# Performance work log

Hardware: AMD Instinct MI355X
Metric: run time of the kernel (lower is better)

## Reference

```python
import jax, jax.numpy as jnp
import numpy as np

N, TD, TE, D = 8, 1024, 2048, 1024

def setup_inputs() -> dict:
    key = jax.random.key(0)
    kq, km, kl = jax.random.split(key, 3)
    queries = jax.random.normal(kq, (N, TD, D), dtype=jnp.float32)
    memory = jax.random.normal(km, (N, TE, D), dtype=jnp.float32)
    # lengths in [1, TE] so no row is fully masked (avoids NaN softmax)
    lengths = jax.random.randint(kl, (N,), 1, TE + 1, dtype=jnp.int32)
    return {"queries": queries, "memory": memory, "lengths": lengths}

def reference(queries, memory, lengths):
    scale = jnp.asarray(np.sqrt(D), dtype=queries.dtype)
    # [N, Td, Te] = bmm(queries, memory^T) / sqrt(D)
    weights = jnp.einsum('ntd,nsd->nts', queries, memory) / scale
    # padding mask: position s is invalid if s >= lengths[n]
    mask = jnp.arange(TE)[None, :] >= lengths[:, None]          # [N, Te]
    weights = jnp.where(mask[:, None, :], -jnp.inf, weights)
    alignments = jax.nn.softmax(weights, axis=-1)               # [N, Td, Te]
    contexts = jnp.einsum('nts,nsd->ntd', alignments, memory)   # [N, Td, D]
    return (contexts, alignments)
```

## Files before the change

### kernel.cpp

```cpp
#include <hip/hip_runtime.h>
#include <hip/hip_bf16.h>

#define NB 8
#define TDIM 1024
#define TEDIM 2048
#define DDIM 1024

typedef __bf16 bf16x8 __attribute__((ext_vector_type(8)));
typedef float f32x4 __attribute__((ext_vector_type(4)));
typedef unsigned short us8 __attribute__((ext_vector_type(8)));

static __device__ __forceinline__ void gld_lds16(const __bf16* g, __bf16* l) {
    __builtin_amdgcn_global_load_lds(
        (const __attribute__((address_space(1))) void*)g,
        (__attribute__((address_space(3))) void*)l,
        16, 0, 0);
}

static __device__ __forceinline__ unsigned short bf16_bits(float f) {
    __bf16 h = (__bf16)f;
    return __builtin_bit_cast(unsigned short, h);
}
static __device__ __forceinline__ float bits_f32(unsigned short u) {
    return (float)__builtin_bit_cast(__bf16, u);
}

__global__ __launch_bounds__(256) void cast_bf16_kernel(
    const float* __restrict__ src, __bf16* __restrict__ dst)
{
    const size_t i = ((size_t)blockIdx.x * 256 + threadIdx.x) * 8;
    float4 a = *reinterpret_cast<const float4*>(&src[i]);
    float4 b = *reinterpret_cast<const float4*>(&src[i + 4]);
    us8 o;
    o[0] = bf16_bits(a.x); o[1] = bf16_bits(a.y);
    o[2] = bf16_bits(a.z); o[3] = bf16_bits(a.w);
    o[4] = bf16_bits(b.x); o[5] = bf16_bits(b.y);
    o[6] = bf16_bits(b.z); o[7] = bf16_bits(b.w);
    *reinterpret_cast<us8*>(&dst[i]) = o;
}

__global__ __launch_bounds__(256) void transpose_cast_m_kernel(
    const float* __restrict__ M, __bf16* __restrict__ Mb,
    __bf16* __restrict__ Mt)
{
    const int n  = blockIdx.z;
    const int s0 = blockIdx.x * 64;
    const int d0 = blockIdx.y * 64;
    const float* Mn  = M  + (size_t)n * TEDIM * DDIM;
    __bf16*      Mbn = Mb + (size_t)n * TEDIM * DDIM;
    __bf16*      Mtn = Mt + (size_t)n * DDIM * TEDIM;

    __shared__ float tile[64][65];
    const int t = threadIdx.x;

    #pragma unroll
    for (int j = 0; j < 4; ++j) {
        const int flat = j * 256 + t;
        const int r  = flat >> 4;
        const int c4 = (flat & 15) * 4;
        float4 v = *reinterpret_cast<const float4*>(
            &Mn[(size_t)(s0 + r) * DDIM + d0 + c4]);
        tile[r][c4 + 0] = v.x; tile[r][c4 + 1] = v.y;
        tile[r][c4 + 2] = v.z; tile[r][c4 + 3] = v.w;
        ushort4 o;
        o.x = bf16_bits(v.x); o.y = bf16_bits(v.y);
        o.z = bf16_bits(v.z); o.w = bf16_bits(v.w);
        *reinterpret_cast<ushort4*>(&Mbn[(size_t)(s0 + r) * DDIM + d0 + c4]) = o;
    }
    __syncthreads();

    const int dr  = t >> 2;
    const int sc0 = (t & 3) * 16;
    us8 o0, o1;
    #pragma unroll
    for (int i = 0; i < 8; ++i)  o0[i] = bf16_bits(tile[sc0 + i][dr]);
    #pragma unroll
    for (int i = 0; i < 8; ++i)  o1[i] = bf16_bits(tile[sc0 + 8 + i][dr]);
    __bf16* dst = &Mtn[(size_t)(d0 + dr) * TEDIM + s0 + sc0];
    *reinterpret_cast<us8*>(dst)     = o0;
    *reinterpret_cast<us8*>(dst + 8) = o1;
}

template<int LDA, int LDB, int LDC, int KDIM, int GX, int GY, int GR,
         bool SCALE, bool OUTBF16>
__global__ __launch_bounds__(256) void gemm_bt_kernel(
    const __bf16* __restrict__ A, const __bf16* __restrict__ B,
    void* __restrict__ Cv)
{
    constexpr int PER_B = GX * GY;
    const int L   = blockIdx.x + GX * (blockIdx.y + GY * blockIdx.z);
    const int n   = L & 7;
    const int rem = L >> 3;
    const int rg  = rem / (GR * GY);
    const int r2  = rem % (GR * GY);
    const int row0 = (rg * GR + (r2 % GR)) * 128;
    const int col0 = (r2 / GR) * 128;

    const __bf16* Ab = A + (size_t)n * GX * 128 * LDA + (size_t)row0 * LDA;
    const __bf16* Bb = B + (size_t)n * GY * 128 * LDB + (size_t)col0 * LDB;

    __shared__ __align__(16) __bf16 As[128 * 32];
    __shared__ __align__(16) __bf16 Bs[128 * 32];

    const int t    = threadIdx.x;
    const int lane = t & 63;
    const int w    = t >> 6;
    const int wr   = (w >> 1) * 64;
    const int wc   = (w & 1) * 64;

    f32x4 acc[4][4] = {};

    for (int k0 = 0; k0 < KDIM; k0 += 32) {
        #pragma unroll
        for (int j = 0; j < 2; ++j) {
            const int tt = j * 256 + t;
            const int r  = tt >> 2;
            const int c  = (tt & 3) * 8;
            gld_lds16(Ab + (size_t)r * LDA + k0 + c, &As[tt * 8]);
            gld_lds16(Bb + (size_t)r * LDB + k0 + c, &Bs[tt * 8]);
        }
        __syncthreads();

        bf16x8 af[4], bfr[4];
        #pragma unroll
        for (int i = 0; i < 4; ++i)
            af[i] = *reinterpret_cast<const bf16x8*>(
                &As[(wr + i * 16 + (lane & 15)) * 32 + (lane >> 4) * 8]);
        #pragma unroll
        for (int j = 0; j < 4; ++j)
            bfr[j] = *reinterpret_cast<const bf16x8*>(
                &Bs[(wc + j * 16 + (lane & 15)) * 32 + (lane >> 4) * 8]);

        #pragma unroll
        for (int i = 0; i < 4; ++i)
            #pragma unroll
            for (int j = 0; j < 4; ++j)
                acc[i][j] = __builtin_amdgcn_mfma_f32_16x16x32_bf16(
                    af[i], bfr[j], acc[i][j], 0, 0, 0);
        __syncthreads();
    }

    const float sc = SCALE ? 0.03125f : 1.0f;
    #pragma unroll
    for (int i = 0; i < 4; ++i) {
        #pragma unroll
        for (int j = 0; j < 4; ++j) {
            const int col   = col0 + wc + j * 16 + (lane & 15);
            const int rbase = row0 + wr + i * 16 + (lane >> 4) * 4;
            #pragma unroll
            for (int r = 0; r < 4; ++r) {
                const size_t idx =
                    (size_t)n * GX * 128 * LDC + (size_t)(rbase + r) * LDC + col;
                if constexpr (OUTBF16)
                    ((__bf16*)Cv)[idx] = (__bf16)(acc[i][j][r] * sc);
                else
                    ((float*)Cv)[idx] = acc[i][j][r] * sc;
            }
        }
    }
}

__global__ __launch_bounds__(256) void softmax_kernel(
    __bf16* __restrict__ P, float* __restrict__ Sout,
    const int* __restrict__ len_p)
{
    const int row = blockIdx.x;
    const int n   = row >> 10;
    const int len = len_p[n];
    __bf16* Pr = P    + (size_t)row * TEDIM;
    float*  Sr = Sout + (size_t)row * TEDIM;

    const int t    = threadIdx.x;
    const int lane = t & 63;
    const int w    = t >> 6;
    const int s0   = t * 8;

    us8 raw = *reinterpret_cast<const us8*>(&Pr[s0]);
    float v[8];
    #pragma unroll
    for (int i = 0; i < 8; ++i) {
        v[i] = bits_f32(raw[i]);
        if (s0 + i >= len) v[i] = -INFINITY;
    }

    float mx = v[0];
    #pragma unroll
    for (int i = 1; i < 8; ++i) mx = fmaxf(mx, v[i]);
    #pragma unroll
    for (int off = 32; off; off >>= 1) mx = fmaxf(mx, __shfl_xor(mx, off));

    __shared__ float redm[4], reds[4];
    if (lane == 0) redm[w] = mx;
    __syncthreads();
    mx = fmaxf(fmaxf(redm[0], redm[1]), fmaxf(redm[2], redm[3]));

    float e[8];
    float sum = 0.f;
    #pragma unroll
    for (int i = 0; i < 8; ++i) { e[i] = __expf(v[i] - mx); sum += e[i]; }
    #pragma unroll
    for (int off = 32; off; off >>= 1) sum += __shfl_xor(sum, off);
    if (lane == 0) reds[w] = sum;
    __syncthreads();
    sum = reds[0] + reds[1] + reds[2] + reds[3];

    const float r = 1.0f / sum;
    float p[8];
    #pragma unroll
    for (int i = 0; i < 8; ++i) p[i] = e[i] * r;

    float4 oa = {p[0], p[1], p[2], p[3]};
    float4 ob = {p[4], p[5], p[6], p[7]};
    *reinterpret_cast<float4*>(&Sr[s0])     = oa;
    *reinterpret_cast<float4*>(&Sr[s0 + 4]) = ob;

    us8 o;
    #pragma unroll
    for (int i = 0; i < 8; ++i) o[i] = bf16_bits(p[i]);
    *reinterpret_cast<us8*>(&Pr[s0]) = o;
}

extern "C" void kernel_launch(void* const* d_in, const int* in_sizes, int n_in,
                              void* d_out, int out_size, void* d_ws, size_t ws_size,
                              hipStream_t stream) {
    const float* Q       = (const float*)d_in[0];
    const float* M       = (const float*)d_in[1];
    const int*   lengths = (const int*)d_in[2];

    float* ctx   = (float*)d_out;
    float* align = ctx + (size_t)NB * TDIM * DDIM;

    __bf16* Qb = (__bf16*)d_ws;
    __bf16* Mb = Qb + (size_t)NB * TDIM * DDIM;
    __bf16* Mt = Mb + (size_t)NB * TEDIM * DDIM;
    __bf16* Pb = Mt + (size_t)NB * DDIM * TEDIM;

    dim3 blk(256);
    cast_bf16_kernel<<<dim3(NB * TDIM * DDIM / (8 * 256)), blk, 0, stream>>>(Q, Qb);
    transpose_cast_m_kernel<<<dim3(TEDIM / 64, DDIM / 64, NB), blk, 0, stream>>>(M, Mb, Mt);
    gemm_bt_kernel<DDIM, DDIM, TEDIM, DDIM, 8, 16, 8, true, true>
        <<<dim3(8, 16, NB), blk, 0, stream>>>(Qb, Mb, (void*)Pb);
    softmax_kernel<<<dim3(NB * TDIM), blk, 0, stream>>>(Pb, align, lengths);
    gemm_bt_kernel<TEDIM, TEDIM, DDIM, TEDIM, 8, 8, 4, false, false>
        <<<dim3(8, 8, NB), blk, 0, stream>>>(Pb, Mt, (void*)ctx);
}
```

Before: 296.3 us.

## Skip masked key positions in transpose, scores and context GEMMs

Uses the per-batch lengths to skip work on padded memory positions. The transpose/cast kernel skips 64-row tiles beyond the length. The scores GEMM returns early for 128-column tiles past the length, with a column remap that interleaves low and high tiles to spread the surviving blocks. The context GEMM limits its K loop to the length rounded up to 32. Correctness depends on softmax overwriting masked positions with -inf and then writing zero probabilities there, because the skipped regions of the workspace are left unwritten.

```diff
diff --git a/kernel.cpp b/kernel.cpp
--- a/kernel.cpp
+++ b/kernel.cpp
@@ -41,10 +41,11 @@
 
 __global__ __launch_bounds__(256) void transpose_cast_m_kernel(
     const float* __restrict__ M, __bf16* __restrict__ Mb,
-    __bf16* __restrict__ Mt)
+    __bf16* __restrict__ Mt, const int* __restrict__ len_p)
 {
     const int n  = blockIdx.z;
     const int s0 = blockIdx.x * 64;
+    if (s0 >= len_p[n]) return;
     const int d0 = blockIdx.y * 64;
     const float* Mn  = M  + (size_t)n * TEDIM * DDIM;
     __bf16*      Mbn = Mb + (size_t)n * TEDIM * DDIM;
@@ -81,23 +82,21 @@
     *reinterpret_cast<us8*>(dst + 8) = o1;
 }
 
-template<int LDA, int LDB, int LDC, int KDIM, int GX, int GY, int GR,
-         bool SCALE, bool OUTBF16>
-__global__ __launch_bounds__(256) void gemm_bt_kernel(
-    const __bf16* __restrict__ A, const __bf16* __restrict__ B,
-    void* __restrict__ Cv)
-{
-    constexpr int PER_B = GX * GY;
-    const int L   = blockIdx.x + GX * (blockIdx.y + GY * blockIdx.z);
-    const int n   = L & 7;
-    const int rem = L >> 3;
-    const int rg  = rem / (GR * GY);
-    const int r2  = rem % (GR * GY);
-    const int row0 = (rg * GR + (r2 % GR)) * 128;
-    const int col0 = (r2 / GR) * 128;
-
-    const __bf16* Ab = A + (size_t)n * GX * 128 * LDA + (size_t)row0 * LDA;
-    const __bf16* Bb = B + (size_t)n * GY * 128 * LDB + (size_t)col0 * LDB;
+__global__ __launch_bounds__(256) void scores_kernel(
+    const __bf16* __restrict__ Qb, const __bf16* __restrict__ Mb,
+    __bf16* __restrict__ Pb, const int* __restrict__ len_p)
+{
+    const int n   = blockIdx.z;
+    const int len = len_p[n];
+    const int xc  = blockIdx.x;
+    const int ct  = (xc < 8) ? xc : 23 - xc;
+    const int col0 = ct * 128;
+    if (col0 >= len) return;
+    const int row0 = blockIdx.y * 128;
+
+    const __bf16* Ab = Qb + (size_t)n * TDIM * DDIM + (size_t)row0 * DDIM;
+    const __bf16* Bb = Mb + (size_t)n * TEDIM * DDIM + (size_t)col0 * DDIM;
+    __bf16*       Cb = Pb + (size_t)n * TDIM * TEDIM;
 
     __shared__ __align__(16) __bf16 As[128 * 32];
     __shared__ __align__(16) __bf16 Bs[128 * 32];
@@ -110,14 +109,14 @@
 
     f32x4 acc[4][4] = {};
 
-    for (int k0 = 0; k0 < KDIM; k0 += 32) {
+    for (int k0 = 0; k0 < DDIM; k0 += 32) {
         #pragma unroll
         for (int j = 0; j < 2; ++j) {
             const int tt = j * 256 + t;
             const int r  = tt >> 2;
             const int c  = (tt & 3) * 8;
-            gld_lds16(Ab + (size_t)r * LDA + k0 + c, &As[tt * 8]);
-            gld_lds16(Bb + (size_t)r * LDB + k0 + c, &Bs[tt * 8]);
+            gld_lds16(Ab + (size_t)r * DDIM + k0 + c, &As[tt * 8]);
+            gld_lds16(Bb + (size_t)r * DDIM + k0 + c, &Bs[tt * 8]);
         }
         __syncthreads();
 
@@ -140,7 +139,6 @@
         __syncthreads();
     }
 
-    const float sc = SCALE ? 0.03125f : 1.0f;
     #pragma unroll
     for (int i = 0; i < 4; ++i) {
         #pragma unroll
@@ -148,14 +146,77 @@
             const int col   = col0 + wc + j * 16 + (lane & 15);
             const int rbase = row0 + wr + i * 16 + (lane >> 4) * 4;
             #pragma unroll
-            for (int r = 0; r < 4; ++r) {
-                const size_t idx =
-                    (size_t)n * GX * 128 * LDC + (size_t)(rbase + r) * LDC + col;
-                if constexpr (OUTBF16)
-                    ((__bf16*)Cv)[idx] = (__bf16)(acc[i][j][r] * sc);
-                else
-                    ((float*)Cv)[idx] = acc[i][j][r] * sc;
-            }
+            for (int r = 0; r < 4; ++r)
+                Cb[(size_t)(rbase + r) * TEDIM + col] =
+                    (__bf16)(acc[i][j][r] * 0.03125f);
+        }
+    }
+}
+
+__global__ __launch_bounds__(256) void contexts_kernel(
+    const __bf16* __restrict__ Pb, const __bf16* __restrict__ Mt,
+    float* __restrict__ C, const int* __restrict__ len_p)
+{
+    const int n    = blockIdx.z;
+    const int len  = len_p[n];
+    const int kmax = (len + 31) & ~31;
+    const int col0 = blockIdx.x * 128;
+    const int row0 = blockIdx.y * 128;
+
+    const __bf16* Ab = Pb + (size_t)n * TDIM * TEDIM + (size_t)row0 * TEDIM;
+    const __bf16* Bb = Mt + (size_t)n * DDIM * TEDIM + (size_t)col0 * TEDIM;
+    float*        Cb = C  + (size_t)n * TDIM * DDIM;
+
+    __shared__ __align__(16) __bf16 As[128 * 32];
+    __shared__ __align__(16) __bf16 Bs[128 * 32];
+
+    const int t    = threadIdx.x;
+    const int lane = t & 63;
+    const int w    = t >> 6;
+    const int wr   = (w >> 1) * 64;
+    const int wc   = (w & 1) * 64;
+
+    f32x4 acc[4][4] = {};
+
+    for (int k0 = 0; k0 < kmax; k0 += 32) {
+        #pragma unroll
+        for (int j = 0; j < 2; ++j) {
+            const int tt = j * 256 + t;
+            const int r  = tt >> 2;
+            const int c  = (tt & 3) * 8;
+            gld_lds16(Ab + (size_t)r * TEDIM + k0 + c, &As[tt * 8]);
+            gld_lds16(Bb + (size_t)r * TEDIM + k0 + c, &Bs[tt * 8]);
+        }
+        __syncthreads();
+
+        bf16x8 af[4], bfr[4];
+        #pragma unroll
+        for (int i = 0; i < 4; ++i)
+            af[i] = *reinterpret_cast<const bf16x8*>(
+                &As[(wr + i * 16 + (lane & 15)) * 32 + (lane >> 4) * 8]);
+        #pragma unroll
+        for (int j = 0; j < 4; ++j)
+            bfr[j] = *reinterpret_cast<const bf16x8*>(
+                &Bs[(wc + j * 16 + (lane & 15)) * 32 + (lane >> 4) * 8]);
+
+        #pragma unroll
+        for (int i = 0; i < 4; ++i)
+            #pragma unroll
+            for (int j = 0; j < 4; ++j)
+                acc[i][j] = __builtin_amdgcn_mfma_f32_16x16x32_bf16(
+                    af[i], bfr[j], acc[i][j], 0, 0, 0);
+        __syncthreads();
+    }
+
+    #pragma unroll
+    for (int i = 0; i < 4; ++i) {
+        #pragma unroll
+        for (int j = 0; j < 4; ++j) {
+            const int col   = col0 + wc + j * 16 + (lane & 15);
+            const int rbase = row0 + wr + i * 16 + (lane >> 4) * 4;
+            #pragma unroll
+            for (int r = 0; r < 4; ++r)
+                Cb[(size_t)(rbase + r) * DDIM + col] = acc[i][j][r];
         }
     }
 }
@@ -237,10 +298,10 @@
 
     dim3 blk(256);
     cast_bf16_kernel<<<dim3(NB * TDIM * DDIM / (8 * 256)), blk, 0, stream>>>(Q, Qb);
-    transpose_cast_m_kernel<<<dim3(TEDIM / 64, DDIM / 64, NB), blk, 0, stream>>>(M, Mb, Mt);
-    gemm_bt_kernel<DDIM, DDIM, TEDIM, DDIM, 8, 16, 8, true, true>
-        <<<dim3(8, 16, NB), blk, 0, stream>>>(Qb, Mb, (void*)Pb);
+    transpose_cast_m_kernel<<<dim3(TEDIM / 64, DDIM / 64, NB), blk, 0, stream>>>(
+        M, Mb, Mt, lengths);
+    scores_kernel<<<dim3(16, TDIM / 128, NB), blk, 0, stream>>>(Qb, Mb, Pb, lengths);
     softmax_kernel<<<dim3(NB * TDIM), blk, 0, stream>>>(Pb, align, lengths);
-    gemm_bt_kernel<TEDIM, TEDIM, DDIM, TEDIM, 8, 8, 4, false, false>
-        <<<dim3(8, 8, NB), blk, 0, stream>>>(Pb, Mt, (void*)ctx);
-}
+    contexts_kernel<<<dim3(DDIM / 128, TDIM / 128, NB), blk, 0, stream>>>(
+        Pb, Mt, ctx, lengths);
+}
```

After: 288.0 us. 1.03x faster.

## Skip masked key tiles by sequence length and widen GEMM K-tile with swizzled LDS

Applied to the files above, without the earlier changes.

Uses each batch's length to skip work past the valid key range. The first GEMM skips column tiles beyond the length, the second GEMM bounds its K loop to the length rounded up to 64, and both the prepass and the softmax skip loading or writing masked regions. The Q cast and the M transpose are merged into one prepass launch. The GEMM K-step grows from 32 to 64 with an XOR-swizzled LDS layout to reduce bank conflicts and barrier count. Columns beyond the length are left unwritten, so correctness depends on the softmax treating them as masked and the second GEMM never reading past klim.

```diff
diff --git a/kernel.cpp b/kernel.cpp
--- a/kernel.cpp
+++ b/kernel.cpp
@@ -25,33 +25,41 @@
     return (float)__builtin_bit_cast(__bf16, u);
 }
 
-__global__ __launch_bounds__(256) void cast_bf16_kernel(
-    const float* __restrict__ src, __bf16* __restrict__ dst)
+__global__ __launch_bounds__(256) void prepass_kernel(
+    const float* __restrict__ Q, const float* __restrict__ M,
+    __bf16* __restrict__ Qb, __bf16* __restrict__ Mb, __bf16* __restrict__ Mt,
+    const int* __restrict__ len_p)
 {
-    const size_t i = ((size_t)blockIdx.x * 256 + threadIdx.x) * 8;
-    float4 a = *reinterpret_cast<const float4*>(&src[i]);
-    float4 b = *reinterpret_cast<const float4*>(&src[i + 4]);
-    us8 o;
-    o[0] = bf16_bits(a.x); o[1] = bf16_bits(a.y);
-    o[2] = bf16_bits(a.z); o[3] = bf16_bits(a.w);
-    o[4] = bf16_bits(b.x); o[5] = bf16_bits(b.y);
-    o[6] = bf16_bits(b.z); o[7] = bf16_bits(b.w);
-    *reinterpret_cast<us8*>(&dst[i]) = o;
-}
-
-__global__ __launch_bounds__(256) void transpose_cast_m_kernel(
-    const float* __restrict__ M, __bf16* __restrict__ Mb,
-    __bf16* __restrict__ Mt)
-{
-    const int n  = blockIdx.z;
+    const int z = blockIdx.z;
+    const int t = threadIdx.x;
+
+    if (z >= NB) {
+        const int flat = (z - NB) * 512 + blockIdx.y * 32 + blockIdx.x;
+        const size_t base = (size_t)flat * 8192 + (size_t)t * 8;
+        #pragma unroll
+        for (int c = 0; c < 4; ++c) {
+            const size_t i = base + (size_t)c * 2048;
+            float4 a = *reinterpret_cast<const float4*>(&Q[i]);
+            float4 b = *reinterpret_cast<const float4*>(&Q[i + 4]);
+            us8 o;
+            o[0] = bf16_bits(a.x); o[1] = bf16_bits(a.y);
+            o[2] = bf16_bits(a.z); o[3] = bf16_bits(a.w);
+            o[4] = bf16_bits(b.x); o[5] = bf16_bits(b.y);
+            o[6] = bf16_bits(b.z); o[7] = bf16_bits(b.w);
+            *reinterpret_cast<us8*>(&Qb[i]) = o;
+        }
+        return;
+    }
+
+    const int n  = z;
     const int s0 = blockIdx.x * 64;
+    if (s0 >= len_p[n]) return;
     const int d0 = blockIdx.y * 64;
     const float* Mn  = M  + (size_t)n * TEDIM * DDIM;
     __bf16*      Mbn = Mb + (size_t)n * TEDIM * DDIM;
     __bf16*      Mtn = Mt + (size_t)n * DDIM * TEDIM;
 
     __shared__ float tile[64][65];
-    const int t = threadIdx.x;
 
     #pragma unroll
     for (int j = 0; j < 4; ++j) {
@@ -81,26 +89,31 @@
     *reinterpret_cast<us8*>(dst + 8) = o1;
 }
 
-template<int LDA, int LDB, int LDC, int KDIM, int GX, int GY, int GR,
-         bool SCALE, bool OUTBF16>
-__global__ __launch_bounds__(256) void gemm_bt_kernel(
+template<int LDA, int LDB, int LDC, int KDIM, long SA, long SB, long SC,
+         bool COLPAIR, bool SCALE, bool OUTBF16, bool KBOUND>
+__global__ __launch_bounds__(256) void gemm_kernel(
     const __bf16* __restrict__ A, const __bf16* __restrict__ B,
-    void* __restrict__ Cv)
+    void* __restrict__ Cv, const int* __restrict__ len_p)
 {
-    constexpr int PER_B = GX * GY;
-    const int L   = blockIdx.x + GX * (blockIdx.y + GY * blockIdx.z);
-    const int n   = L & 7;
-    const int rem = L >> 3;
-    const int rg  = rem / (GR * GY);
-    const int r2  = rem % (GR * GY);
-    const int row0 = (rg * GR + (r2 % GR)) * 128;
-    const int col0 = (r2 / GR) * 128;
-
-    const __bf16* Ab = A + (size_t)n * GX * 128 * LDA + (size_t)row0 * LDA;
-    const __bf16* Bb = B + (size_t)n * GY * 128 * LDB + (size_t)col0 * LDB;
-
-    __shared__ __align__(16) __bf16 As[128 * 32];
-    __shared__ __align__(16) __bf16 Bs[128 * 32];
+    const int n   = blockIdx.z;
+    const int len = len_p[n];
+    int ct;
+    if constexpr (COLPAIR) {
+        const int xc = blockIdx.x;
+        ct = (xc < 8) ? xc : 23 - xc;
+        if (ct * 128 >= len) return;
+    } else {
+        ct = blockIdx.x;
+    }
+    const int col0 = ct * 128;
+    const int row0 = blockIdx.y * 128;
+    const int klim = KBOUND ? ((len + 63) & ~63) : KDIM;
+
+    const __bf16* Ab = A + (size_t)n * SA + (size_t)row0 * LDA;
+    const __bf16* Bb = B + (size_t)n * SB + (size_t)col0 * LDB;
+
+    __shared__ __align__(16) __bf16 As[128 * 64];
+    __shared__ __align__(16) __bf16 Bs[128 * 64];
 
     const int t    = threadIdx.x;
     const int lane = t & 63;
@@ -110,33 +123,41 @@
 
     f32x4 acc[4][4] = {};
 
-    for (int k0 = 0; k0 < KDIM; k0 += 32) {
-        #pragma unroll
-        for (int j = 0; j < 2; ++j) {
-            const int tt = j * 256 + t;
-            const int r  = tt >> 2;
-            const int c  = (tt & 3) * 8;
-            gld_lds16(Ab + (size_t)r * LDA + k0 + c, &As[tt * 8]);
-            gld_lds16(Bb + (size_t)r * LDB + k0 + c, &Bs[tt * 8]);
+    for (int k0 = 0; k0 < klim; k0 += 64) {
+        #pragma unroll
+        for (int j = 0; j < 4; ++j) {
+            const int slot = j * 256 + t;
+            const int r    = slot >> 3;
+            const int cg   = (slot & 7) ^ (r & 7);
+            gld_lds16(Ab + (size_t)r * LDA + k0 + cg * 8, &As[slot * 8]);
+            gld_lds16(Bb + (size_t)r * LDB + k0 + cg * 8, &Bs[slot * 8]);
         }
         __syncthreads();
 
-        bf16x8 af[4], bfr[4];
-        #pragma unroll
-        for (int i = 0; i < 4; ++i)
-            af[i] = *reinterpret_cast<const bf16x8*>(
-                &As[(wr + i * 16 + (lane & 15)) * 32 + (lane >> 4) * 8]);
-        #pragma unroll
-        for (int j = 0; j < 4; ++j)
-            bfr[j] = *reinterpret_cast<const bf16x8*>(
-                &Bs[(wc + j * 16 + (lane & 15)) * 32 + (lane >> 4) * 8]);
-
-        #pragma unroll
-        for (int i = 0; i < 4; ++i)
+        bf16x8 af[2][4], bfr[2][4];
+        #pragma unroll
+        for (int kk = 0; kk < 2; ++kk) {
             #pragma unroll
-            for (int j = 0; j < 4; ++j)
-                acc[i][j] = __builtin_amdgcn_mfma_f32_16x16x32_bf16(
-                    af[i], bfr[j], acc[i][j], 0, 0, 0);
+            for (int i = 0; i < 4; ++i) {
+                const int rowa = wr + i * 16 + (lane & 15);
+                const int ca   = (kk * 4 + (lane >> 4)) ^ (rowa & 7);
+                af[kk][i] = *reinterpret_cast<const bf16x8*>(
+                    &As[rowa * 64 + ca * 8]);
+                const int rowb = wc + i * 16 + (lane & 15);
+                const int cb   = (kk * 4 + (lane >> 4)) ^ (rowb & 7);
+                bfr[kk][i] = *reinterpret_cast<const bf16x8*>(
+                    &Bs[rowb * 64 + cb * 8]);
+            }
+        }
+
+        #pragma unroll
+        for (int kk = 0; kk < 2; ++kk)
+            #pragma unroll
+            for (int i = 0; i < 4; ++i)
+                #pragma unroll
+                for (int j = 0; j < 4; ++j)
+                    acc[i][j] = __builtin_amdgcn_mfma_f32_16x16x32_bf16(
+                        af[kk][i], bfr[kk][j], acc[i][j], 0, 0, 0);
         __syncthreads();
     }
 
@@ -149,8 +170,7 @@
             const int rbase = row0 + wr + i * 16 + (lane >> 4) * 4;
             #pragma unroll
             for (int r = 0; r < 4; ++r) {
-                const size_t idx =
-                    (size_t)n * GX * 128 * LDC + (size_t)(rbase + r) * LDC + col;
+                const size_t idx = (size_t)n * SC + (size_t)(rbase + r) * LDC + col;
                 if constexpr (OUTBF16)
                     ((__bf16*)Cv)[idx] = (__bf16)(acc[i][j][r] * sc);
                 else
@@ -167,6 +187,7 @@
     const int row = blockIdx.x;
     const int n   = row >> 10;
     const int len = len_p[n];
+    const int kmax = (len + 63) & ~63;
     __bf16* Pr = P    + (size_t)row * TEDIM;
     float*  Sr = Sout + (size_t)row * TEDIM;
 
@@ -175,12 +196,17 @@
     const int w    = t >> 6;
     const int s0   = t * 8;
 
-    us8 raw = *reinterpret_cast<const us8*>(&Pr[s0]);
     float v[8];
-    #pragma unroll
-    for (int i = 0; i < 8; ++i) {
-        v[i] = bits_f32(raw[i]);
-        if (s0 + i >= len) v[i] = -INFINITY;
+    if (s0 < len) {
+        us8 raw = *reinterpret_cast<const us8*>(&Pr[s0]);
+        #pragma unroll
+        for (int i = 0; i < 8; ++i) {
+            v[i] = bits_f32(raw[i]);
+            if (s0 + i >= len) v[i] = -INFINITY;
+        }
+    } else {
+        #pragma unroll
+        for (int i = 0; i < 8; ++i) v[i] = -INFINITY;
     }
 
     float mx = v[0];
@@ -214,10 +240,12 @@
     *reinterpret_cast<float4*>(&Sr[s0])     = oa;
     *reinterpret_cast<float4*>(&Sr[s0 + 4]) = ob;
 
-    us8 o;
-    #pragma unroll
-    for (int i = 0; i < 8; ++i) o[i] = bf16_bits(p[i]);
-    *reinterpret_cast<us8*>(&Pr[s0]) = o;
+    if (s0 < kmax) {
+        us8 o;
+        #pragma unroll
+        for (int i = 0; i < 8; ++i) o[i] = bf16_bits(p[i]);
+        *reinterpret_cast<us8*>(&Pr[s0]) = o;
+    }
 }
 
 extern "C" void kernel_launch(void* const* d_in, const int* in_sizes, int n_in,
@@ -236,11 +264,14 @@
     __bf16* Pb = Mt + (size_t)NB * DDIM * TEDIM;
 
     dim3 blk(256);
-    cast_bf16_kernel<<<dim3(NB * TDIM * DDIM / (8 * 256)), blk, 0, stream>>>(Q, Qb);
-    transpose_cast_m_kernel<<<dim3(TEDIM / 64, DDIM / 64, NB), blk, 0, stream>>>(M, Mb, Mt);
-    gemm_bt_kernel<DDIM, DDIM, TEDIM, DDIM, 8, 16, 8, true, true>
-        <<<dim3(8, 16, NB), blk, 0, stream>>>(Qb, Mb, (void*)Pb);
+    prepass_kernel<<<dim3(32, 16, 10), blk, 0, stream>>>(Q, M, Qb, Mb, Mt, lengths);
+    gemm_kernel<DDIM, DDIM, TEDIM, DDIM,
+                (long)TDIM * DDIM, (long)TEDIM * DDIM, (long)TDIM * TEDIM,
+                true, true, true, false>
+        <<<dim3(16, TDIM / 128, NB), blk, 0, stream>>>(Qb, Mb, (void*)Pb, lengths);
     softmax_kernel<<<dim3(NB * TDIM), blk, 0, stream>>>(Pb, align, lengths);
-    gemm_bt_kernel<TEDIM, TEDIM, DDIM, TEDIM, 8, 8, 4, false, false>
-        <<<dim3(8, 8, NB), blk, 0, stream>>>(Pb, Mt, (void*)ctx);
-}
+    gemm_kernel<TEDIM, TEDIM, DDIM, TEDIM,
+                (long)TDIM * TEDIM, (long)DDIM * TEDIM, (long)TDIM * DDIM,
+                false, false, false, true>
+        <<<dim3(DDIM / 128, TDIM / 128, NB), blk, 0, stream>>>(Pb, Mt, (void*)ctx, lengths);
+}
```

After: 273.1 us. 7.8% less time.
